# Optimization experiments

Hardware: AMD Instinct MI355X
Metric: run time of the kernel (lower is better)

## Reference

```python
import jax, jax.numpy as jnp
import numpy as np

B, I, H, MS, M = 8192, 1024, 1024, 64, 16
TAU = 1.0


def setup_inputs() -> dict:
    key = jax.random.key(0)
    ks = jax.random.split(key, 24)
    s = 0.02
    eps = 1e-6
    return {
        "x": jax.random.normal(ks[0], (B, I), jnp.float32),
        "h": jax.random.normal(ks[1], (B, H), jnp.float32),
        "c": jax.random.normal(ks[2], (B, H), jnp.float32),
        "memory": jax.random.normal(ks[3], (B, M, MS), jnp.float32),
        "u_gs": jax.random.uniform(ks[4], (B, M), jnp.float32, eps, 1.0 - eps),
        "u_a": jax.random.uniform(ks[5], (B, 1), jnp.float32, eps, 1.0 - eps),
        "u_b": jax.random.uniform(ks[6], (B, 1), jnp.float32, eps, 1.0 - eps),
        # pre-concatenated gate weights, matching torch.cat((W_x2*, W_h2*, W_c2*), 0)
        "W_i": jax.random.normal(ks[7], (I + 2 * H, H), jnp.float32) * s,
        "b_i": jnp.zeros((H,), jnp.float32),
        "W_f": jax.random.normal(ks[8], (I + 2 * H, H), jnp.float32) * s,
        "b_f": jnp.ones((H,), jnp.float32),
        "W_o": jax.random.normal(ks[9], (I + 2 * H, H), jnp.float32) * s,
        "b_o": jnp.zeros((H,), jnp.float32),
        "W_cand": jax.random.normal(ks[10], (I + H, H), jnp.float32) * s,
        "b_cand": jnp.zeros((H,), jnp.float32),
        "W_m": jax.random.normal(ks[11], (H, MS), jnp.float32) * s,
        "b_m": jnp.zeros((MS,), jnp.float32),
        "w_a_h": jax.random.normal(ks[12], (H, 1), jnp.float32) * s,
        "w_a_x": jax.random.normal(ks[13], (I, 1), jnp.float32) * s,
        "w_a_r": jax.random.normal(ks[14], (MS, 1), jnp.float32) * s,
        "w_b_h": jax.random.normal(ks[15], (H, 1), jnp.float32) * s,
        "w_b_x": jax.random.normal(ks[16], (I, 1), jnp.float32) * s,
        "w_b_r": jax.random.normal(ks[17], (MS, 1), jnp.float32) * s,
    }


def reference(x, h, c, memory, u_gs, u_a, u_b,
              W_i, b_i, W_f, b_f, W_o, b_o, W_cand, b_cand,
              W_m, b_m, w_a_h, w_a_x, w_a_r, w_b_h, w_b_x, w_b_r):
    # LSTM-style gates with peephole c in the concatenated input
    xhc = jnp.concatenate([x, h, c], axis=1)            # [B, I+2H]
    i = jax.nn.sigmoid(xhc @ W_i + b_i)
    f = jax.nn.sigmoid(xhc @ W_f + b_f)
    cp = jnp.tanh(jnp.concatenate([x, h], axis=1) @ W_cand + b_cand)
    c_new = f * c + i * cp
    o = jax.nn.sigmoid(jnp.concatenate([x, h, c_new], axis=1) @ W_o + b_o)
    h_new = o * jnp.tanh(c_new)

    # memory-slot attention with Gumbel-softmax sampling
    micro = h_new @ W_m + b_m                           # [B, MS]
    logits = jnp.einsum('bmk,bk->bm', memory, micro)    # [B, M]
    g = -jnp.log(-jnp.log(u_gs))                        # Gumbel(0,1)
    attn = jax.nn.softmax((logits + g) / TAU, axis=-1)  # sampled_locations
    sampled = jnp.einsum('bmk,bm->bk', memory, attn) + 1.0  # [B, MS]

    # gumbel-sigmoid (binary concrete) for alpha / beta
    la = jnp.log(u_a) - jnp.log1p(-u_a)
    lb = jnp.log(u_b) - jnp.log1p(-u_b)
    alpha = jax.nn.sigmoid((h_new @ w_a_h + x @ w_a_x + sampled @ w_a_r + la) / TAU)
    beta = jax.nn.sigmoid((h_new @ w_b_h + x @ w_b_x + sampled @ w_b_r + lb) / TAU)

    # [B, 2H+2]
    return jnp.concatenate([h_new, c_new, alpha, beta], axis=1)
```

## Files before the change

### kernel.cpp

```cpp
#include <hip/hip_runtime.h>

typedef __bf16 bfrag __attribute__((ext_vector_type(8)));
typedef float f32x4 __attribute__((ext_vector_type(4)));

#define GLDS16(g, l) __builtin_amdgcn_global_load_lds( \
    (__attribute__((address_space(1))) void*)(g),      \
    (__attribute__((address_space(3))) void*)(l), 16, 0, 0)

__device__ __forceinline__ float bf2f(ushort u) {
    return __uint_as_float(((unsigned)u) << 16);
}
__device__ __forceinline__ ushort f2bf(float f) {
    unsigned u = __float_as_uint(f);
    u += 0x7fff + ((u >> 16) & 1);
    return (ushort)(u >> 16);
}
__device__ __forceinline__ float sigmoidf_(float v) {
    return 1.0f / (1.0f + expf(-v));
}

__global__ __launch_bounds__(256) void k_castcat(const float* __restrict__ x,
                                                 const float* __restrict__ h,
                                                 const float* __restrict__ c,
                                                 ushort* __restrict__ xhcb) {
    int idx = blockIdx.x * 256 + threadIdx.x;
    int row = idx / 384;
    int c8 = (idx - row * 384) * 8;
    const float* s = (c8 < 1024) ? &x[(size_t)row * 1024 + c8]
                   : (c8 < 2048) ? &h[(size_t)row * 1024 + (c8 - 1024)]
                                 : &c[(size_t)row * 1024 + (c8 - 2048)];
    float4 a = *(const float4*)s;
    float4 b = *(const float4*)(s + 4);
    ushort tmp[8] = {f2bf(a.x), f2bf(a.y), f2bf(a.z), f2bf(a.w),
                     f2bf(b.x), f2bf(b.y), f2bf(b.z), f2bf(b.w)};
    *(uint4*)&xhcb[(size_t)idx * 8] = *(uint4*)tmp;
}

__global__ __launch_bounds__(256) void k_transW(const float* __restrict__ src,
                                                ushort* __restrict__ dst, int dst_ld) {
    __shared__ float tile[64][65];
    int k0 = blockIdx.x * 64, n0 = blockIdx.y * 64;
    int t = threadIdx.x;
    int c4 = (t & 15) * 4;
    int r = t >> 4;
#pragma unroll
    for (int i = 0; i < 4; ++i) {
        int rr = r + i * 16;
        float4 v = *(const float4*)&src[(size_t)(k0 + rr) * 1024 + n0 + c4];
        tile[rr][c4 + 0] = v.x; tile[rr][c4 + 1] = v.y;
        tile[rr][c4 + 2] = v.z; tile[rr][c4 + 3] = v.w;
    }
    __syncthreads();
    int kk8 = (t & 7) * 8;
    int nn = t >> 3;
#pragma unroll
    for (int i = 0; i < 2; ++i) {
        int n = nn + i * 32;
        ushort tmp[8];
#pragma unroll
        for (int j = 0; j < 8; ++j) tmp[j] = f2bf(tile[kk8 + j][n]);
        *(uint4*)&dst[(size_t)(n0 + n) * dst_ld + k0 + kk8] = *(uint4*)tmp;
    }
}

__global__ void k_biasf(const float* bi, const float* bf_, const float* bc,
                        const float* bo, float* dst) {
    int t = blockIdx.x * 256 + threadIdx.x;
    int g = t >> 10, n = t & 1023;
    const float* s = (g == 0) ? bi : (g == 1) ? bf_ : (g == 2) ? bc : bo;
    dst[t] = s[n];
}

__global__ __launch_bounds__(256) void k_gemm1(const ushort* __restrict__ xhcb,
                                               const ushort* __restrict__ WT,
                                               const float* __restrict__ bias,
                                               ushort* __restrict__ Pre) {
    __shared__ __align__(16) ushort As[128 * 32];
    __shared__ __align__(16) ushort Bs[128 * 32];
    int t = threadIdx.x;
    int m0 = blockIdx.x * 128, n0 = blockIdx.y * 128;
    int Kext = (n0 >= 2048) ? 2048 : 3072;
    int w = t >> 6, l = t & 63;
    int wm = (w & 1) * 64, wn = (w >> 1) * 64;
    int lane16 = l & 15, quad = l >> 4;
    int sr = t >> 2;
    int sk = (t & 3) * 8;
    f32x4 acc[4][4] = {};

    for (int k0 = 0; k0 < Kext; k0 += 32) {
        GLDS16(xhcb + (size_t)(m0 + sr) * 3072 + k0 + sk,       As + t * 8);
        GLDS16(xhcb + (size_t)(m0 + sr + 64) * 3072 + k0 + sk,  As + 2048 + t * 8);
        GLDS16(WT + (size_t)(n0 + sr) * 3072 + k0 + sk,         Bs + t * 8);
        GLDS16(WT + (size_t)(n0 + sr + 64) * 3072 + k0 + sk,    Bs + 2048 + t * 8);
        __syncthreads();
        bfrag af[4], bfr[4];
#pragma unroll
        for (int i = 0; i < 4; ++i) {
            af[i]  = *(const bfrag*)&As[(wm + i * 16 + lane16) * 32 + quad * 8];
            bfr[i] = *(const bfrag*)&Bs[(wn + i * 16 + lane16) * 32 + quad * 8];
        }
#pragma unroll
        for (int i = 0; i < 4; ++i)
#pragma unroll
            for (int j = 0; j < 4; ++j)
                acc[i][j] = __builtin_amdgcn_mfma_f32_16x16x32_bf16(af[i], bfr[j], acc[i][j], 0, 0, 0);
        __syncthreads();
    }
#pragma unroll
    for (int i = 0; i < 4; ++i) {
#pragma unroll
        for (int j = 0; j < 4; ++j) {
            int col = n0 + wn + j * 16 + lane16;
            float bv = bias[col];
            int rbase = m0 + wm + i * 16 + quad * 4;
#pragma unroll
            for (int r = 0; r < 4; ++r)
                Pre[(size_t)(rbase + r) * 4096 + col] = f2bf(acc[i][j][r] + bv);
        }
    }
}

__global__ __launch_bounds__(256) void k_cnew(const ushort* __restrict__ Pre,
                                              const float* __restrict__ cin,
                                              ushort* __restrict__ Cnewb,
                                              float* __restrict__ out) {
    int idx8 = blockIdx.x * 256 + threadIdx.x;
    int b = idx8 >> 7;
    int n8 = (idx8 & 127) * 8;
    uint4 vi = *(const uint4*)(Pre + (size_t)b * 4096 + n8);
    uint4 vf = *(const uint4*)(Pre + (size_t)b * 4096 + 1024 + n8);
    uint4 vc = *(const uint4*)(Pre + (size_t)b * 4096 + 2048 + n8);
    float4 c0 = *(const float4*)(cin + (size_t)b * 1024 + n8);
    float4 c1 = *(const float4*)(cin + (size_t)b * 1024 + n8 + 4);
    const ushort* pi = (const ushort*)&vi;
    const ushort* pf = (const ushort*)&vf;
    const ushort* pc = (const ushort*)&vc;
    float cv[8] = {c0.x, c0.y, c0.z, c0.w, c1.x, c1.y, c1.z, c1.w};
    float cn[8];
    ushort cb[8];
#pragma unroll
    for (int j = 0; j < 8; ++j) {
        float iv = sigmoidf_(bf2f(pi[j]));
        float fv = sigmoidf_(bf2f(pf[j]));
        float cp = tanhf(bf2f(pc[j]));
        cn[j] = fv * cv[j] + iv * cp;
        cb[j] = f2bf(cn[j]);
    }
    *(uint4*)(Cnewb + (size_t)b * 1024 + n8) = *(uint4*)cb;
    float* orow = out + (size_t)b * 2050 + 1024 + n8;
#pragma unroll
    for (int j = 0; j < 4; ++j)
        *(float2*)(orow + j * 2) = make_float2(cn[j * 2], cn[j * 2 + 1]);
}

__global__ __launch_bounds__(256) void k_gemm2(const ushort* __restrict__ Cnewb,
                                               const ushort* __restrict__ WoCT,
                                               const ushort* __restrict__ Pre,
                                               float* __restrict__ out) {
    __shared__ __align__(16) ushort As[128 * 32];
    __shared__ __align__(16) ushort Bs[128 * 32];
    int t = threadIdx.x;
    int m0 = blockIdx.x * 128, n0 = blockIdx.y * 128;
    int w = t >> 6, l = t & 63;
    int wm = (w & 1) * 64, wn = (w >> 1) * 64;
    int lane16 = l & 15, quad = l >> 4;
    int sr = t >> 2;
    int sk = (t & 3) * 8;
    f32x4 acc[4][4] = {};

    for (int k0 = 0; k0 < 1024; k0 += 32) {
        GLDS16(Cnewb + (size_t)(m0 + sr) * 1024 + k0 + sk,       As + t * 8);
        GLDS16(Cnewb + (size_t)(m0 + sr + 64) * 1024 + k0 + sk,  As + 2048 + t * 8);
        GLDS16(WoCT + (size_t)(n0 + sr) * 1024 + k0 + sk,        Bs + t * 8);
        GLDS16(WoCT + (size_t)(n0 + sr + 64) * 1024 + k0 + sk,   Bs + 2048 + t * 8);
        __syncthreads();
        bfrag af[4], bfr[4];
#pragma unroll
        for (int i = 0; i < 4; ++i) {
            af[i]  = *(const bfrag*)&As[(wm + i * 16 + lane16) * 32 + quad * 8];
            bfr[i] = *(const bfrag*)&Bs[(wn + i * 16 + lane16) * 32 + quad * 8];
        }
#pragma unroll
        for (int i = 0; i < 4; ++i)
#pragma unroll
            for (int j = 0; j < 4; ++j)
                acc[i][j] = __builtin_amdgcn_mfma_f32_16x16x32_bf16(af[i], bfr[j], acc[i][j], 0, 0, 0);
        __syncthreads();
    }
#pragma unroll
    for (int i = 0; i < 4; ++i) {
#pragma unroll
        for (int j = 0; j < 4; ++j) {
            int col = n0 + wn + j * 16 + lane16;
            int rbase = m0 + wm + i * 16 + quad * 4;
#pragma unroll
            for (int r = 0; r < 4; ++r) {
                int row = rbase + r;
                float opre = acc[i][j][r] + bf2f(Pre[(size_t)row * 4096 + 3072 + col]);
                float o = sigmoidf_(opre);
                float cnv = bf2f(Cnewb[(size_t)row * 1024 + col]);
                out[(size_t)row * 2050 + col] = o * tanhf(cnv);
            }
        }
    }
}

__global__ __launch_bounds__(256) void k_attn(
    const float* __restrict__ outr, const float* __restrict__ x,
    const float* __restrict__ memory, const float* __restrict__ u_gs,
    const float* __restrict__ u_a, const float* __restrict__ u_b,
    const float* __restrict__ W_m, const float* __restrict__ b_m,
    const float* __restrict__ w_a_h, const float* __restrict__ w_a_x,
    const float* __restrict__ w_a_r, const float* __restrict__ w_b_h,
    const float* __restrict__ w_b_x, const float* __restrict__ w_b_r,
    float* __restrict__ out) {
    __shared__ float sWm[128 * 64];
    __shared__ float sH[16 * 128];
    __shared__ float sMicro[16 * 64];
    __shared__ float sAttn[16 * 16];
    __shared__ float sSamp[16 * 64];

    int b0 = blockIdx.x * 16;
    int t = threadIdx.x;
    int j = t & 63, g = t >> 6;

    float acc[4] = {0.f, 0.f, 0.f, 0.f};
    for (int kc = 0; kc < 1024; kc += 128) {
#pragma unroll
        for (int i = 0; i < 8; ++i) {
            int e = (i * 256 + t) * 4;
            *(float4*)&sWm[e] = *(const float4*)&W_m[(size_t)(kc + (e >> 6)) * 64 + (e & 63)];
        }
        {
            int r = t >> 4, cc = (t & 15) * 8;
            const float* src = &outr[(size_t)(b0 + r) * 2050 + kc + cc];
            float* d = &sH[r * 128 + cc];
#pragma unroll
            for (int q = 0; q < 4; ++q) {
                float2 v = *(const float2*)(src + q * 2);
                d[q * 2] = v.x; d[q * 2 + 1] = v.y;
            }
        }
        __syncthreads();
        for (int k = 0; k < 128; ++k) {
            float wm = sWm[k * 64 + j];
#pragma unroll
            for (int q = 0; q < 4; ++q)
                acc[q] += sH[(g * 4 + q) * 128 + k] * wm;
        }
        __syncthreads();
    }
    {
        float bm = b_m[j];
#pragma unroll
        for (int q = 0; q < 4; ++q) sMicro[(g * 4 + q) * 64 + j] = acc[q] + bm;
    }
    __syncthreads();

    {
        int r = t >> 4, m = t & 15;
        const float* mem = memory + (size_t)(b0 + r) * 1024 + m * 64;
        float lg = 0.f;
        for (int k = 0; k < 64; ++k) lg += mem[k] * sMicro[r * 64 + k];
        float u = u_gs[(b0 + r) * 16 + m];
        float z = lg + (-logf(-logf(u)));
        float zm = z;
        for (int off = 8; off; off >>= 1) zm = fmaxf(zm, __shfl_xor(zm, off, 16));
        float p = expf(z - zm);
        float ps = p;
        for (int off = 8; off; off >>= 1) ps += __shfl_xor(ps, off, 16);
        sAttn[r * 16 + m] = p / ps;
    }
    __syncthreads();

#pragma unroll
    for (int q = 0; q < 4; ++q) {
        int r = g * 4 + q;
        const float* mem = memory + (size_t)(b0 + r) * 1024 + j;
        float s = 0.f;
#pragma unroll
        for (int m = 0; m < 16; ++m) s += sAttn[r * 16 + m] * mem[m * 64];
        sSamp[r * 64 + j] = s + 1.0f;
    }
    __syncthreads();

    {
        int r = t >> 4, s16 = t & 15;
        size_t hoff = (size_t)(b0 + r) * 2050;
        size_t xoff = (size_t)(b0 + r) * 1024;
        float za = 0.f, zb = 0.f;
        for (int kk = 0; kk < 64; ++kk) {
            int k = s16 + kk * 16;
            float hv = outr[hoff + k];
            float xv = x[xoff + k];
            za += hv * w_a_h[k] + xv * w_a_x[k];
            zb += hv * w_b_h[k] + xv * w_b_x[k];
        }
#pragma unroll
        for (int k = s16 * 4; k < s16 * 4 + 4; ++k) {
            float sv = sSamp[r * 64 + k];
            za += sv * w_a_r[k];
            zb += sv * w_b_r[k];
        }
        for (int off = 8; off; off >>= 1) {
            za += __shfl_xor(za, off, 16);
            zb += __shfl_xor(zb, off, 16);
        }
        if (s16 == 0) {
            float ua = u_a[b0 + r];
            float ub = u_b[b0 + r];
            float la = logf(ua) - log1pf(-ua);
            float lb = logf(ub) - log1pf(-ub);
            out[(size_t)(b0 + r) * 2050 + 2048] = sigmoidf_(za + la);
            out[(size_t)(b0 + r) * 2050 + 2049] = sigmoidf_(zb + lb);
        }
    }
}

extern "C" void kernel_launch(void* const* d_in, const int* in_sizes, int n_in,
                              void* d_out, int out_size, void* d_ws, size_t ws_size,
                              hipStream_t stream) {
    const float* x      = (const float*)d_in[0];
    const float* h      = (const float*)d_in[1];
    const float* c      = (const float*)d_in[2];
    const float* memory = (const float*)d_in[3];
    const float* u_gs   = (const float*)d_in[4];
    const float* u_a    = (const float*)d_in[5];
    const float* u_b    = (const float*)d_in[6];
    const float* W_i    = (const float*)d_in[7];
    const float* b_i    = (const float*)d_in[8];
    const float* W_f    = (const float*)d_in[9];
    const float* b_f    = (const float*)d_in[10];
    const float* W_o    = (const float*)d_in[11];
    const float* b_o    = (const float*)d_in[12];
    const float* W_cand = (const float*)d_in[13];
    const float* b_cand = (const float*)d_in[14];
    const float* W_m    = (const float*)d_in[15];
    const float* b_m    = (const float*)d_in[16];
    const float* w_a_h  = (const float*)d_in[17];
    const float* w_a_x  = (const float*)d_in[18];
    const float* w_a_r  = (const float*)d_in[19];
    const float* w_b_h  = (const float*)d_in[20];
    const float* w_b_x  = (const float*)d_in[21];
    const float* w_b_r  = (const float*)d_in[22];
    float* out = (float*)d_out;

    char* ws = (char*)d_ws;
    ushort* WT    = (ushort*)(ws);
    ushort* WoCT  = (ushort*)(ws + 25165824);
    ushort* Pre   = (ushort*)(ws + 27262976);
    ushort* xhcb  = (ushort*)(ws + 94371840);
    float*  Biasf = (float*)(ws + 144703488);
    ushort* Cnewb = xhcb;

    k_castcat<<<12288, 256, 0, stream>>>(x, h, c, xhcb);
    k_transW<<<dim3(48, 16), 256, 0, stream>>>(W_i, WT, 3072);
    k_transW<<<dim3(48, 16), 256, 0, stream>>>(W_f, WT + (size_t)1024 * 3072, 3072);
    k_transW<<<dim3(32, 16), 256, 0, stream>>>(W_cand, WT + (size_t)2048 * 3072, 3072);
    k_transW<<<dim3(32, 16), 256, 0, stream>>>(W_o, WT + (size_t)3072 * 3072, 3072);
    k_transW<<<dim3(16, 16), 256, 0, stream>>>(W_o + (size_t)2048 * 1024, WoCT, 1024);
    k_biasf<<<16, 256, 0, stream>>>(b_i, b_f, b_cand, b_o, Biasf);

    k_gemm1<<<dim3(64, 32), 256, 0, stream>>>(xhcb, WT, Biasf, Pre);
    k_cnew<<<4096, 256, 0, stream>>>(Pre, c, Cnewb, out);
    k_gemm2<<<dim3(64, 8), 256, 0, stream>>>(Cnewb, WoCT, Pre, out);
    k_attn<<<512, 256, 0, stream>>>(out, x, memory, u_gs, u_a, u_b, W_m, b_m,
                                    w_a_h, w_a_x, w_a_r, w_b_h, w_b_x, w_b_r, out);
}
```

Baseline: 580.4 us.

## Swizzle GEMM LDS tiles, merge weight transposes, and use MFMA for micro projection

Applies an XOR swizzle to the LDS layout in both GEMMs so fragment reads avoid bank conflicts. Merges the five weight-transpose launches plus a new W_m transpose into one table-driven kernel, reducing launch overhead. gemm2 now also writes h_new as bf16, and the attention kernel computes h_new @ W_m with MFMA instead of scalar FP32 loops, plus vectorized memory loads. This lowers the precision of the micro projection to bf16.

```diff
diff --git a/kernel.cpp b/kernel.cpp
--- a/kernel.cpp
+++ b/kernel.cpp
@@ -36,17 +36,29 @@
     *(uint4*)&xhcb[(size_t)idx * 8] = *(uint4*)tmp;
 }
 
-__global__ __launch_bounds__(256) void k_transW(const float* __restrict__ src,
-                                                ushort* __restrict__ dst, int dst_ld) {
+struct TD { const float* src; ushort* dst; int src_ld; int dst_ld; int ktiles; int off; };
+struct TA { TD d[6]; };
+
+__global__ __launch_bounds__(256) void k_transAll(TA a) {
     __shared__ float tile[64][65];
-    int k0 = blockIdx.x * 64, n0 = blockIdx.y * 64;
+    int bid = blockIdx.x;
+    int ri = 0;
+#pragma unroll
+    for (int i = 1; i < 6; ++i) ri = (bid >= a.d[i].off) ? i : ri;
+    const float* src = a.d[ri].src;
+    ushort* dst = a.d[ri].dst;
+    int src_ld = a.d[ri].src_ld, dst_ld = a.d[ri].dst_ld;
+    int local = bid - a.d[ri].off;
+    int bx = local % a.d[ri].ktiles;
+    int by = local / a.d[ri].ktiles;
+    int k0 = bx * 64, n0 = by * 64;
     int t = threadIdx.x;
     int c4 = (t & 15) * 4;
     int r = t >> 4;
 #pragma unroll
     for (int i = 0; i < 4; ++i) {
         int rr = r + i * 16;
-        float4 v = *(const float4*)&src[(size_t)(k0 + rr) * 1024 + n0 + c4];
+        float4 v = *(const float4*)&src[(size_t)(k0 + rr) * src_ld + n0 + c4];
         tile[rr][c4 + 0] = v.x; tile[rr][c4 + 1] = v.y;
         tile[rr][c4 + 2] = v.z; tile[rr][c4 + 3] = v.w;
     }
@@ -84,20 +96,21 @@
     int wm = (w & 1) * 64, wn = (w >> 1) * 64;
     int lane16 = l & 15, quad = l >> 4;
     int sr = t >> 2;
-    int sk = (t & 3) * 8;
+    int sko = (((t & 3) ^ ((sr >> 1) & 3))) * 8;
+    int sw8 = ((lane16 >> 1) & 3) * 8;
     f32x4 acc[4][4] = {};
 
     for (int k0 = 0; k0 < Kext; k0 += 32) {
-        GLDS16(xhcb + (size_t)(m0 + sr) * 3072 + k0 + sk,       As + t * 8);
-        GLDS16(xhcb + (size_t)(m0 + sr + 64) * 3072 + k0 + sk,  As + 2048 + t * 8);
-        GLDS16(WT + (size_t)(n0 + sr) * 3072 + k0 + sk,         Bs + t * 8);
-        GLDS16(WT + (size_t)(n0 + sr + 64) * 3072 + k0 + sk,    Bs + 2048 + t * 8);
+        GLDS16(xhcb + (size_t)(m0 + sr) * 3072 + k0 + sko,       As + t * 8);
+        GLDS16(xhcb + (size_t)(m0 + sr + 64) * 3072 + k0 + sko,  As + 2048 + t * 8);
+        GLDS16(WT + (size_t)(n0 + sr) * 3072 + k0 + sko,         Bs + t * 8);
+        GLDS16(WT + (size_t)(n0 + sr + 64) * 3072 + k0 + sko,    Bs + 2048 + t * 8);
         __syncthreads();
         bfrag af[4], bfr[4];
 #pragma unroll
         for (int i = 0; i < 4; ++i) {
-            af[i]  = *(const bfrag*)&As[(wm + i * 16 + lane16) * 32 + quad * 8];
-            bfr[i] = *(const bfrag*)&Bs[(wn + i * 16 + lane16) * 32 + quad * 8];
+            af[i]  = *(const bfrag*)&As[(wm + i * 16 + lane16) * 32 + ((quad * 8) ^ sw8)];
+            bfr[i] = *(const bfrag*)&Bs[(wn + i * 16 + lane16) * 32 + ((quad * 8) ^ sw8)];
         }
 #pragma unroll
         for (int i = 0; i < 4; ++i)
@@ -156,6 +169,7 @@
 __global__ __launch_bounds__(256) void k_gemm2(const ushort* __restrict__ Cnewb,
                                                const ushort* __restrict__ WoCT,
                                                const ushort* __restrict__ Pre,
+                                               ushort* __restrict__ Hnewb,
                                                float* __restrict__ out) {
     __shared__ __align__(16) ushort As[128 * 32];
     __shared__ __align__(16) ushort Bs[128 * 32];
@@ -165,20 +179,21 @@
     int wm = (w & 1) * 64, wn = (w >> 1) * 64;
     int lane16 = l & 15, quad = l >> 4;
     int sr = t >> 2;
-    int sk = (t & 3) * 8;
+    int sko = (((t & 3) ^ ((sr >> 1) & 3))) * 8;
+    int sw8 = ((lane16 >> 1) & 3) * 8;
     f32x4 acc[4][4] = {};
 
     for (int k0 = 0; k0 < 1024; k0 += 32) {
-        GLDS16(Cnewb + (size_t)(m0 + sr) * 1024 + k0 + sk,       As + t * 8);
-        GLDS16(Cnewb + (size_t)(m0 + sr + 64) * 1024 + k0 + sk,  As + 2048 + t * 8);
-        GLDS16(WoCT + (size_t)(n0 + sr) * 1024 + k0 + sk,        Bs + t * 8);
-        GLDS16(WoCT + (size_t)(n0 + sr + 64) * 1024 + k0 + sk,   Bs + 2048 + t * 8);
+        GLDS16(Cnewb + (size_t)(m0 + sr) * 1024 + k0 + sko,       As + t * 8);
+        GLDS16(Cnewb + (size_t)(m0 + sr + 64) * 1024 + k0 + sko,  As + 2048 + t * 8);
+        GLDS16(WoCT + (size_t)(n0 + sr) * 1024 + k0 + sko,        Bs + t * 8);
+        GLDS16(WoCT + (size_t)(n0 + sr + 64) * 1024 + k0 + sko,   Bs + 2048 + t * 8);
         __syncthreads();
         bfrag af[4], bfr[4];
 #pragma unroll
         for (int i = 0; i < 4; ++i) {
-            af[i]  = *(const bfrag*)&As[(wm + i * 16 + lane16) * 32 + quad * 8];
-            bfr[i] = *(const bfrag*)&Bs[(wn + i * 16 + lane16) * 32 + quad * 8];
+            af[i]  = *(const bfrag*)&As[(wm + i * 16 + lane16) * 32 + ((quad * 8) ^ sw8)];
+            bfr[i] = *(const bfrag*)&Bs[(wn + i * 16 + lane16) * 32 + ((quad * 8) ^ sw8)];
         }
 #pragma unroll
         for (int i = 0; i < 4; ++i)
@@ -199,71 +214,62 @@
                 float opre = acc[i][j][r] + bf2f(Pre[(size_t)row * 4096 + 3072 + col]);
                 float o = sigmoidf_(opre);
                 float cnv = bf2f(Cnewb[(size_t)row * 1024 + col]);
-                out[(size_t)row * 2050 + col] = o * tanhf(cnv);
+                float hv = o * tanhf(cnv);
+                Hnewb[(size_t)row * 1024 + col] = f2bf(hv);
+                out[(size_t)row * 2050 + col] = hv;
             }
         }
     }
 }
 
 __global__ __launch_bounds__(256) void k_attn(
-    const float* __restrict__ outr, const float* __restrict__ x,
-    const float* __restrict__ memory, const float* __restrict__ u_gs,
-    const float* __restrict__ u_a, const float* __restrict__ u_b,
-    const float* __restrict__ W_m, const float* __restrict__ b_m,
+    const ushort* __restrict__ Hnewb, const float* __restrict__ outr,
+    const float* __restrict__ x, const float* __restrict__ memory,
+    const float* __restrict__ u_gs, const float* __restrict__ u_a,
+    const float* __restrict__ u_b, const ushort* __restrict__ WmT,
+    const float* __restrict__ b_m,
     const float* __restrict__ w_a_h, const float* __restrict__ w_a_x,
     const float* __restrict__ w_a_r, const float* __restrict__ w_b_h,
     const float* __restrict__ w_b_x, const float* __restrict__ w_b_r,
     float* __restrict__ out) {
-    __shared__ float sWm[128 * 64];
-    __shared__ float sH[16 * 128];
     __shared__ float sMicro[16 * 64];
     __shared__ float sAttn[16 * 16];
     __shared__ float sSamp[16 * 64];
 
     int b0 = blockIdx.x * 16;
     int t = threadIdx.x;
-    int j = t & 63, g = t >> 6;
-
-    float acc[4] = {0.f, 0.f, 0.f, 0.f};
-    for (int kc = 0; kc < 1024; kc += 128) {
-#pragma unroll
-        for (int i = 0; i < 8; ++i) {
-            int e = (i * 256 + t) * 4;
-            *(float4*)&sWm[e] = *(const float4*)&W_m[(size_t)(kc + (e >> 6)) * 64 + (e & 63)];
-        }
-        {
-            int r = t >> 4, cc = (t & 15) * 8;
-            const float* src = &outr[(size_t)(b0 + r) * 2050 + kc + cc];
-            float* d = &sH[r * 128 + cc];
-#pragma unroll
-            for (int q = 0; q < 4; ++q) {
-                float2 v = *(const float2*)(src + q * 2);
-                d[q * 2] = v.x; d[q * 2 + 1] = v.y;
-            }
-        }
-        __syncthreads();
-        for (int k = 0; k < 128; ++k) {
-            float wm = sWm[k * 64 + j];
-#pragma unroll
-            for (int q = 0; q < 4; ++q)
-                acc[q] += sH[(g * 4 + q) * 128 + k] * wm;
-        }
-        __syncthreads();
-    }
+    int w = t >> 6, l = t & 63;
+    int lane16 = l & 15, quad = l >> 4;
+
     {
-        float bm = b_m[j];
-#pragma unroll
-        for (int q = 0; q < 4; ++q) sMicro[(g * 4 + q) * 64 + j] = acc[q] + bm;
+        f32x4 acc = {0.f, 0.f, 0.f, 0.f};
+        const ushort* Ab = Hnewb + (size_t)(b0 + lane16) * 1024 + quad * 8;
+        const ushort* Bb = WmT + (size_t)(w * 16 + lane16) * 1024 + quad * 8;
+#pragma unroll 4
+        for (int k0 = 0; k0 < 1024; k0 += 32) {
+            bfrag av = *(const bfrag*)(Ab + k0);
+            bfrag bv = *(const bfrag*)(Bb + k0);
+            acc = __builtin_amdgcn_mfma_f32_16x16x32_bf16(av, bv, acc, 0, 0, 0);
+        }
+        float bm = b_m[w * 16 + lane16];
+#pragma unroll
+        for (int r = 0; r < 4; ++r)
+            sMicro[(quad * 4 + r) * 64 + w * 16 + lane16] = acc[r] + bm;
     }
     __syncthreads();
 
     {
         int r = t >> 4, m = t & 15;
-        const float* mem = memory + (size_t)(b0 + r) * 1024 + m * 64;
+        const float4* mem4 = (const float4*)(memory + (size_t)(b0 + r) * 1024 + m * 64);
         float lg = 0.f;
-        for (int k = 0; k < 64; ++k) lg += mem[k] * sMicro[r * 64 + k];
+#pragma unroll
+        for (int k4 = 0; k4 < 16; ++k4) {
+            float4 mv = mem4[k4];
+            const float* sm = &sMicro[r * 64 + k4 * 4];
+            lg += mv.x * sm[0] + mv.y * sm[1] + mv.z * sm[2] + mv.w * sm[3];
+        }
         float u = u_gs[(b0 + r) * 16 + m];
-        float z = lg + (-logf(-logf(u)));
+        float z = lg - logf(-logf(u));
         float zm = z;
         for (int off = 8; off; off >>= 1) zm = fmaxf(zm, __shfl_xor(zm, off, 16));
         float p = expf(z - zm);
@@ -275,12 +281,12 @@
 
 #pragma unroll
     for (int q = 0; q < 4; ++q) {
-        int r = g * 4 + q;
-        const float* mem = memory + (size_t)(b0 + r) * 1024 + j;
+        int r = w * 4 + q;
+        const float* mem = memory + (size_t)(b0 + r) * 1024 + l;
         float s = 0.f;
 #pragma unroll
         for (int m = 0; m < 16; ++m) s += sAttn[r * 16 + m] * mem[m * 64];
-        sSamp[r * 64 + j] = s + 1.0f;
+        sSamp[r * 64 + l] = s + 1.0f;
     }
     __syncthreads();
 
@@ -351,19 +357,25 @@
     ushort* Pre   = (ushort*)(ws + 27262976);
     ushort* xhcb  = (ushort*)(ws + 94371840);
     float*  Biasf = (float*)(ws + 144703488);
+    ushort* WmT   = (ushort*)(ws + 144719872);
     ushort* Cnewb = xhcb;
+    ushort* Hnewb = WT;
 
     k_castcat<<<12288, 256, 0, stream>>>(x, h, c, xhcb);
-    k_transW<<<dim3(48, 16), 256, 0, stream>>>(W_i, WT, 3072);
-    k_transW<<<dim3(48, 16), 256, 0, stream>>>(W_f, WT + (size_t)1024 * 3072, 3072);
-    k_transW<<<dim3(32, 16), 256, 0, stream>>>(W_cand, WT + (size_t)2048 * 3072, 3072);
-    k_transW<<<dim3(32, 16), 256, 0, stream>>>(W_o, WT + (size_t)3072 * 3072, 3072);
-    k_transW<<<dim3(16, 16), 256, 0, stream>>>(W_o + (size_t)2048 * 1024, WoCT, 1024);
+
+    TA ta;
+    ta.d[0] = {W_i,                      WT,                        1024, 3072, 48, 0};
+    ta.d[1] = {W_f,                      WT + (size_t)1024 * 3072,  1024, 3072, 48, 768};
+    ta.d[2] = {W_cand,                   WT + (size_t)2048 * 3072,  1024, 3072, 32, 1536};
+    ta.d[3] = {W_o,                      WT + (size_t)3072 * 3072,  1024, 3072, 48, 2048};
+    ta.d[4] = {W_o + (size_t)2048 * 1024, WoCT,                     1024, 1024, 16, 2816};
+    ta.d[5] = {W_m,                      WmT,                         64, 1024, 16, 3072};
+    k_transAll<<<3088, 256, 0, stream>>>(ta);
     k_biasf<<<16, 256, 0, stream>>>(b_i, b_f, b_cand, b_o, Biasf);
 
     k_gemm1<<<dim3(64, 32), 256, 0, stream>>>(xhcb, WT, Biasf, Pre);
     k_cnew<<<4096, 256, 0, stream>>>(Pre, c, Cnewb, out);
-    k_gemm2<<<dim3(64, 8), 256, 0, stream>>>(Cnewb, WoCT, Pre, out);
-    k_attn<<<512, 256, 0, stream>>>(out, x, memory, u_gs, u_a, u_b, W_m, b_m,
+    k_gemm2<<<dim3(64, 8), 256, 0, stream>>>(Cnewb, WoCT, Pre, Hnewb, out);
+    k_attn<<<512, 256, 0, stream>>>(Hnewb, out, x, memory, u_gs, u_a, u_b, WmT, b_m,
                                     w_a_h, w_a_x, w_a_r, w_b_h, w_b_x, w_b_r, out);
 }
```

Result: no change. 572.0 us (-1.4%).
